# Performance work log

Hardware: AMD Instinct MI355X
Metric: run time of the kernel (lower is better)

Reference implementation:

```python
import jax, jax.numpy as jnp
import numpy as np

N_NODES = 256
N_SECRETS = 64
N_INPUTS = 16      # per-node source-node inputs
N_SECDEP = 8       # per-node secret-dependency columns
ENTRIES = 3 + N_INPUTS + N_SECDEP  # 27
ACTION_SIZE = 4096
BATCH = 8192
STATE_DIM = N_NODES + N_SECRETS + 2  # 322


def _build_index_matrix() -> np.ndarray:
    """idx[i] = column indices of `state` concatenated for node i, mirroring split()."""
    rng = np.random.default_rng(1234)
    idx = np.empty((N_NODES, ENTRIES), dtype=np.int32)
    g0 = N_NODES + N_SECRETS  # first of the two global columns
    for i in range(N_NODES):
        src = rng.integers(0, N_NODES, size=N_INPUTS)           # inputs[j].sourceNodeIndex
        sec = N_NODES + rng.choice(N_SECRETS, size=N_SECDEP, replace=False)  # secrIndex[i]
        idx[i] = np.concatenate(([i, g0, g0 + 1], src, np.sort(sec)))
    return idx


def setup_inputs() -> dict:
    key = jax.random.key(0)
    k1, k2, k3, k4 = jax.random.split(key, 4)
    state = jax.random.normal(k1, (BATCH, STATE_DIM), dtype=jnp.float32)
    # per-node Linear(ENTRIES, 1): weight [N, E], bias [N]
    bound = 1.0 / np.sqrt(ENTRIES)
    W = jax.random.uniform(k2, (N_NODES, ENTRIES), jnp.float32, -bound, bound)
    b = jax.random.uniform(k3, (N_NODES,), jnp.float32, -bound, bound)
    # final Linear(N_NODES, ACTION_SIZE, bias=False): weight [A, N]
    bf = 1.0 / np.sqrt(N_NODES)
    Wf = jax.random.uniform(k4, (ACTION_SIZE, N_NODES), jnp.float32, -bf, bf)
    idx = jnp.asarray(_build_index_matrix())
    return {"state": state, "W": W, "b": b, "Wf": Wf, "idx": idx}


def reference(state, W, b, Wf, idx):
    # split(): per-node gather of ENTRIES columns -> [B, N, E]
    gathered = jnp.take(state, idx, axis=1)
    # per-node tiny Linear + tanh -> [B, N]
    y = jnp.tanh(jnp.einsum("bne,ne->bn", gathered, W) + b)
    # final linear (no bias), scaled sigmoid -> [B, A]
    return 500.0 * jax.nn.sigmoid(jnp.einsum("bn,an->ba", y, Wf))
```

## Files before the change

### kernel.cpp

```cpp
#include <hip/hip_runtime.h>
#include <hip/hip_bf16.h>
#include <cmath>

#define ENTRIES 27
#define ACTION  4096
#define BATCH   8192
#define SDIM    322
#define KPAD    352
#define NNODES  256

typedef unsigned short u16;
typedef u16 u16x4 __attribute__((ext_vector_type(4)));
typedef u16 u16x8 __attribute__((ext_vector_type(8)));
typedef __bf16 bf16x8 __attribute__((ext_vector_type(8)));
typedef float floatx4 __attribute__((ext_vector_type(4)));

__device__ __forceinline__ u16 f2bf(float f) {
    unsigned u = __builtin_bit_cast(unsigned, f);
    unsigned r = (u + 0x7FFFu + ((u >> 16) & 1u)) >> 16;
    return (u16)r;
}

__device__ __forceinline__ void gl_lds16(const u16* g, u16* l) {
    __builtin_amdgcn_global_load_lds(
        (const __attribute__((address_space(1))) unsigned int*)g,
        (__attribute__((address_space(3))) unsigned int*)l, 16, 0, 0);
}

__global__ __launch_bounds__(256) void build_wg(
    const float* __restrict__ W, const int* __restrict__ idx,
    u16* __restrict__ wg)
{
    __shared__ float rows[32 * KPAD];
    const int tid = threadIdx.x;
    for (int i = tid; i < 32 * KPAD; i += 256) rows[i] = 0.f;
    __syncthreads();
    if (tid < 32) {
        const int n = blockIdx.x * 32 + tid;
        for (int e = 0; e < ENTRIES; e++)
            rows[tid * KPAD + idx[n * ENTRIES + e]] += W[n * ENTRIES + e];
    }
    __syncthreads();
    for (int i = tid; i < 32 * KPAD; i += 256)
        wg[(size_t)blockIdx.x * 32 * KPAD + i] = f2bf(rows[i]);
}

__global__ __launch_bounds__(256) void conv_state(
    const float* __restrict__ s, u16* __restrict__ o)
{
    const int i = blockIdx.x * 256 + threadIdx.x;
    const int b = i / KPAD;
    const int c = i - b * KPAD;
    float v = (c < SDIM) ? s[(size_t)b * SDIM + c] : 0.f;
    o[i] = f2bf(v);
}

__global__ __launch_bounds__(256) void conv_wf(
    const float* __restrict__ wf, u16* __restrict__ out)
{
    const int i0 = (blockIdx.x * 256 + threadIdx.x) * 4;
    floatx4 v = *(const floatx4*)(wf + i0);
    u16x4 r;
    r.x = f2bf(v.x); r.y = f2bf(v.y); r.z = f2bf(v.z); r.w = f2bf(v.w);
    *(u16x4*)(out + i0) = r;
}

template<int KDIM, int EPI>
__global__ __launch_bounds__(256) void gemm_mfma(
    const u16* __restrict__ A, const u16* __restrict__ B,
    void* __restrict__ outp, const float* __restrict__ bias)
{
    __shared__ u16 As[128 * 32];
    __shared__ u16 Bs[128 * 32];

    const int bm   = blockIdx.x;
    const int bn   = blockIdx.y;
    const int tid  = threadIdx.x;
    const int lane = tid & 63;
    const int wave = tid >> 6;
    const int wm   = wave & 1;
    const int wn   = wave >> 1;
    const int l15  = lane & 15;
    const int koff = (lane >> 4) << 3;

    floatx4 acc[4][4];
#pragma unroll
    for (int mi = 0; mi < 4; mi++)
#pragma unroll
        for (int ni = 0; ni < 4; ni++)
            acc[mi][ni] = (floatx4){0.f, 0.f, 0.f, 0.f};

    const int srow = wave * 32 + (lane >> 2);
    const int ksub = (lane & 3) << 3;
    const u16* ga = A + ((size_t)bm * 128 + srow) * KDIM + ksub;
    const u16* gb = B + ((size_t)bn * 128 + srow) * KDIM + ksub;
    u16* la = &As[(wave * 32) * 32];
    u16* lb = &Bs[(wave * 32) * 32];

    for (int kk = 0; kk < KDIM; kk += 32) {
        __syncthreads();
        gl_lds16(ga + kk,                  la);
        gl_lds16(ga + kk + 16 * KDIM,      la + 16 * 32);
        gl_lds16(gb + kk,                  lb);
        gl_lds16(gb + kk + 16 * KDIM,      lb + 16 * 32);
        __syncthreads();

        bf16x8 af[4], bf[4];
#pragma unroll
        for (int mi = 0; mi < 4; mi++)
            af[mi] = __builtin_bit_cast(bf16x8,
                *(const u16x8*)&As[((wm << 6) + (mi << 4) + l15) * 32 + koff]);
#pragma unroll
        for (int ni = 0; ni < 4; ni++)
            bf[ni] = __builtin_bit_cast(bf16x8,
                *(const u16x8*)&Bs[((wn << 6) + (ni << 4) + l15) * 32 + koff]);

#pragma unroll
        for (int mi = 0; mi < 4; mi++)
#pragma unroll
            for (int ni = 0; ni < 4; ni++)
                acc[mi][ni] = __builtin_amdgcn_mfma_f32_16x16x32_bf16(
                    af[mi], bf[ni], acc[mi][ni], 0, 0, 0);
    }

    const int r0 = (lane >> 4) << 2;
    float bv[4];
    if (EPI == 1) {
#pragma unroll
        for (int ni = 0; ni < 4; ni++)
            bv[ni] = bias[bn * 128 + wn * 64 + ni * 16 + l15];
    }
#pragma unroll
    for (int mi = 0; mi < 4; mi++) {
#pragma unroll
        for (int ni = 0; ni < 4; ni++) {
            const int row = bm * 128 + wm * 64 + mi * 16 + r0;
            const int col = bn * 128 + wn * 64 + ni * 16 + l15;
#pragma unroll
            for (int r = 0; r < 4; r++) {
                float v = acc[mi][ni][r];
                if (EPI == 0) {
                    ((float*)outp)[(size_t)(row + r) * ACTION + col] =
                        500.0f / (1.0f + __expf(-v));
                } else {
                    ((u16*)outp)[(size_t)(row + r) * NNODES + col] =
                        f2bf(tanhf(v + bv[ni]));
                }
            }
        }
    }
}

extern "C" void kernel_launch(void* const* d_in, const int* in_sizes, int n_in,
                              void* d_out, int out_size, void* d_ws, size_t ws_size,
                              hipStream_t stream) {
    const float* state = (const float*)d_in[0];
    const float* W     = (const float*)d_in[1];
    const float* b     = (const float*)d_in[2];
    const float* Wf    = (const float*)d_in[3];
    const int*   idx   = (const int*)  d_in[4];
    float* out = (float*)d_out;

    u16* sbf = (u16*)d_ws;
    u16* wg  = sbf + (size_t)BATCH * KPAD;
    u16* y   = wg  + (size_t)NNODES * KPAD;
    u16* wfb = y   + (size_t)BATCH * NNODES;

    build_wg  <<<NNODES / 32, 256, 0, stream>>>(W, idx, wg);
    conv_state<<<BATCH * KPAD / 256, 256, 0, stream>>>(state, sbf);
    conv_wf   <<<ACTION * NNODES / 1024, 256, 0, stream>>>(Wf, wfb);
    gemm_mfma<KPAD, 1><<<dim3(BATCH / 128, NNODES / 128), 256, 0, stream>>>(
        sbf, wg, (void*)y, b);
    gemm_mfma<256, 0><<<dim3(BATCH / 128, ACTION / 128), 256, 0, stream>>>(
        y, wfb, (void*)out, nullptr);
}
```

Baseline: 190.5 us.

## Parallelize weight build, vectorize state conversion, narrow first GEMM tile, fast tanh/sigmoid

The dense weight build now gives one thread per (node, entry) pair and uses LDS atomics, with 8 nodes per block instead of 32 serial threads. State conversion handles four columns per thread with a vectorized store. The GEMM gains a BN template so the first GEMM uses 64-wide N tiles, doubling its block count to fill more CUs, and the loader is generalized into chunks. The epilogues use fast-math exp/divide forms for tanh and sigmoid, which are slightly less accurate.

```diff
diff --git a/kernel.cpp b/kernel.cpp
--- a/kernel.cpp
+++ b/kernel.cpp
@@ -21,6 +21,13 @@
     return (u16)r;
 }
 
+__device__ __forceinline__ float sig500(float v) {
+    return __fdividef(500.0f, 1.0f + __expf(-v));
+}
+__device__ __forceinline__ float ftanh(float x) {
+    return 1.0f - __fdividef(2.0f, __expf(2.0f * x) + 1.0f);
+}
+
 __device__ __forceinline__ void gl_lds16(const u16* g, u16* l) {
     __builtin_amdgcn_global_load_lds(
         (const __attribute__((address_space(1))) unsigned int*)g,
@@ -31,28 +38,36 @@
     const float* __restrict__ W, const int* __restrict__ idx,
     u16* __restrict__ wg)
 {
-    __shared__ float rows[32 * KPAD];
+    __shared__ float rows[8 * KPAD];
     const int tid = threadIdx.x;
-    for (int i = tid; i < 32 * KPAD; i += 256) rows[i] = 0.f;
+    for (int i = tid; i < 8 * KPAD; i += 256) rows[i] = 0.f;
     __syncthreads();
-    if (tid < 32) {
-        const int n = blockIdx.x * 32 + tid;
-        for (int e = 0; e < ENTRIES; e++)
-            rows[tid * KPAD + idx[n * ENTRIES + e]] += W[n * ENTRIES + e];
+    if (tid < 8 * ENTRIES) {
+        const int nl = tid / ENTRIES;
+        const int e  = tid - nl * ENTRIES;
+        const int n  = blockIdx.x * 8 + nl;
+        atomicAdd(&rows[nl * KPAD + idx[n * ENTRIES + e]], W[n * ENTRIES + e]);
     }
     __syncthreads();
-    for (int i = tid; i < 32 * KPAD; i += 256)
-        wg[(size_t)blockIdx.x * 32 * KPAD + i] = f2bf(rows[i]);
+    for (int i = tid; i < 8 * KPAD; i += 256)
+        wg[(size_t)blockIdx.x * 8 * KPAD + i] = f2bf(rows[i]);
 }
 
 __global__ __launch_bounds__(256) void conv_state(
     const float* __restrict__ s, u16* __restrict__ o)
 {
-    const int i = blockIdx.x * 256 + threadIdx.x;
-    const int b = i / KPAD;
-    const int c = i - b * KPAD;
-    float v = (c < SDIM) ? s[(size_t)b * SDIM + c] : 0.f;
-    o[i] = f2bf(v);
+    const int t   = blockIdx.x * 256 + threadIdx.x;
+    const int row = t / 88;
+    const int c0  = (t - row * 88) * 4;
+    const float* sp = s + (size_t)row * SDIM;
+    u16x4 r;
+#pragma unroll
+    for (int q = 0; q < 4; q++) {
+        const int c = c0 + q;
+        float v = (c < SDIM) ? sp[c] : 0.f;
+        ((u16*)&r)[q] = f2bf(v);
+    }
+    *(u16x4*)(o + (size_t)row * KPAD + c0) = r;
 }
 
 __global__ __launch_bounds__(256) void conv_wf(
@@ -65,13 +80,18 @@
     *(u16x4*)(out + i0) = r;
 }
 
-template<int KDIM, int EPI>
+template<int KDIM, int EPI, int BN>
 __global__ __launch_bounds__(256) void gemm_mfma(
     const u16* __restrict__ A, const u16* __restrict__ B,
     void* __restrict__ outp, const float* __restrict__ bias)
 {
+    constexpr int NI  = BN / 32;
+    constexpr int WN  = BN / 2;
+    constexpr int ACH = 8;
+    constexpr int BCH = BN / 16;
+
     __shared__ u16 As[128 * 32];
-    __shared__ u16 Bs[128 * 32];
+    __shared__ u16 Bs[BN * 32];
 
     const int bm   = blockIdx.x;
     const int bn   = blockIdx.y;
@@ -83,68 +103,70 @@
     const int l15  = lane & 15;
     const int koff = (lane >> 4) << 3;
 
-    floatx4 acc[4][4];
+    floatx4 acc[4][NI];
 #pragma unroll
     for (int mi = 0; mi < 4; mi++)
 #pragma unroll
-        for (int ni = 0; ni < 4; ni++)
+        for (int ni = 0; ni < NI; ni++)
             acc[mi][ni] = (floatx4){0.f, 0.f, 0.f, 0.f};
 
-    const int srow = wave * 32 + (lane >> 2);
-    const int ksub = (lane & 3) << 3;
-    const u16* ga = A + ((size_t)bm * 128 + srow) * KDIM + ksub;
-    const u16* gb = B + ((size_t)bn * 128 + srow) * KDIM + ksub;
-    u16* la = &As[(wave * 32) * 32];
-    u16* lb = &Bs[(wave * 32) * 32];
+    const int crow = lane >> 2;
+    const int ckel = (lane & 3) << 3;
 
     for (int kk = 0; kk < KDIM; kk += 32) {
         __syncthreads();
-        gl_lds16(ga + kk,                  la);
-        gl_lds16(ga + kk + 16 * KDIM,      la + 16 * 32);
-        gl_lds16(gb + kk,                  lb);
-        gl_lds16(gb + kk + 16 * KDIM,      lb + 16 * 32);
+#pragma unroll
+        for (int c = wave; c < ACH + BCH; c += 4) {
+            const bool isA = c < ACH;
+            const int  cr  = isA ? c : c - ACH;
+            const int  row = cr * 16 + crow;
+            const u16* g = isA
+                ? (A + ((size_t)bm * 128 + row) * KDIM + kk + ckel)
+                : (B + ((size_t)bn * BN  + row) * KDIM + kk + ckel);
+            u16* l = isA ? &As[cr * 512] : &Bs[cr * 512];
+            gl_lds16(g, l);
+        }
         __syncthreads();
 
-        bf16x8 af[4], bf[4];
+        bf16x8 af[4], bfg[NI];
 #pragma unroll
         for (int mi = 0; mi < 4; mi++)
             af[mi] = __builtin_bit_cast(bf16x8,
                 *(const u16x8*)&As[((wm << 6) + (mi << 4) + l15) * 32 + koff]);
 #pragma unroll
-        for (int ni = 0; ni < 4; ni++)
-            bf[ni] = __builtin_bit_cast(bf16x8,
-                *(const u16x8*)&Bs[((wn << 6) + (ni << 4) + l15) * 32 + koff]);
+        for (int ni = 0; ni < NI; ni++)
+            bfg[ni] = __builtin_bit_cast(bf16x8,
+                *(const u16x8*)&Bs[(wn * WN + (ni << 4) + l15) * 32 + koff]);
 
 #pragma unroll
         for (int mi = 0; mi < 4; mi++)
 #pragma unroll
-            for (int ni = 0; ni < 4; ni++)
+            for (int ni = 0; ni < NI; ni++)
                 acc[mi][ni] = __builtin_amdgcn_mfma_f32_16x16x32_bf16(
-                    af[mi], bf[ni], acc[mi][ni], 0, 0, 0);
+                    af[mi], bfg[ni], acc[mi][ni], 0, 0, 0);
     }
 
     const int r0 = (lane >> 4) << 2;
-    float bv[4];
+    float bv[NI];
     if (EPI == 1) {
 #pragma unroll
-        for (int ni = 0; ni < 4; ni++)
-            bv[ni] = bias[bn * 128 + wn * 64 + ni * 16 + l15];
+        for (int ni = 0; ni < NI; ni++)
+            bv[ni] = bias[bn * BN + wn * WN + ni * 16 + l15];
     }
 #pragma unroll
     for (int mi = 0; mi < 4; mi++) {
 #pragma unroll
-        for (int ni = 0; ni < 4; ni++) {
+        for (int ni = 0; ni < NI; ni++) {
             const int row = bm * 128 + wm * 64 + mi * 16 + r0;
-            const int col = bn * 128 + wn * 64 + ni * 16 + l15;
+            const int col = bn * BN + wn * WN + ni * 16 + l15;
 #pragma unroll
             for (int r = 0; r < 4; r++) {
                 float v = acc[mi][ni][r];
                 if (EPI == 0) {
-                    ((float*)outp)[(size_t)(row + r) * ACTION + col] =
-                        500.0f / (1.0f + __expf(-v));
+                    ((float*)outp)[(size_t)(row + r) * ACTION + col] = sig500(v);
                 } else {
                     ((u16*)outp)[(size_t)(row + r) * NNODES + col] =
-                        f2bf(tanhf(v + bv[ni]));
+                        f2bf(ftanh(v + bv[ni]));
                 }
             }
         }
@@ -166,11 +188,11 @@
     u16* y   = wg  + (size_t)NNODES * KPAD;
     u16* wfb = y   + (size_t)BATCH * NNODES;
 
-    build_wg  <<<NNODES / 32, 256, 0, stream>>>(W, idx, wg);
-    conv_state<<<BATCH * KPAD / 256, 256, 0, stream>>>(state, sbf);
+    build_wg  <<<NNODES / 8, 256, 0, stream>>>(W, idx, wg);
+    conv_state<<<BATCH * 88 / 256, 256, 0, stream>>>(state, sbf);
     conv_wf   <<<ACTION * NNODES / 1024, 256, 0, stream>>>(Wf, wfb);
-    gemm_mfma<KPAD, 1><<<dim3(BATCH / 128, NNODES / 128), 256, 0, stream>>>(
+    gemm_mfma<KPAD, 1, 64><<<dim3(BATCH / 128, NNODES / 64), 256, 0, stream>>>(
         sbf, wg, (void*)y, b);
-    gemm_mfma<256, 0><<<dim3(BATCH / 128, ACTION / 128), 256, 0, stream>>>(
+    gemm_mfma<256, 0, 128><<<dim3(BATCH / 128, ACTION / 128), 256, 0, stream>>>(
         y, wfb, (void*)out, nullptr);
 }
```

Result: faster. 182.2 us (-4.3%).
